# Kernel tuning notes

Hardware: AMD Instinct MI355X
Metric: run time of the kernel (lower is better)

Reference implementation:

```python
import jax, jax.numpy as jnp
import numpy as np

N_NODES = 50000
N_EDGES = 800000
F_IN = 8
H = 128
N_CLASSES = 2


def _gcn_conv(x, W, b, src, dst, n_nodes):
    # PyG GCNConv: add self-loops, symmetric normalization, aggregate, bias.
    h = x @ W  # [N, H]
    loop = jnp.arange(n_nodes, dtype=src.dtype)
    s = jnp.concatenate([src, loop])  # message sources
    d = jnp.concatenate([dst, loop])  # message targets
    deg = jax.ops.segment_sum(jnp.ones_like(s, dtype=h.dtype), d, num_segments=n_nodes)
    dinv = jnp.where(deg > 0, jax.lax.rsqrt(deg), 0.0)
    norm = dinv[s] * dinv[d]  # [E+N]
    out = jax.ops.segment_sum(h[s] * norm[:, None], d, num_segments=n_nodes)
    return out + b


def setup_inputs() -> dict:
    key = jax.random.key(0)
    ks = jax.random.split(key, 10)
    x = jax.random.normal(ks[0], (N_NODES, F_IN), dtype=jnp.float32)
    edge_index = jax.random.randint(ks[1], (2, N_EDGES), 0, N_NODES, dtype=jnp.int64)

    def glorot(k, shape):
        lim = np.sqrt(6.0 / (shape[0] + shape[1]))
        return jax.random.uniform(k, shape, jnp.float32, -lim, lim)

    return {
        "x": x,
        "W1": glorot(ks[2], (F_IN, H)),
        "b1": jnp.zeros((H,), jnp.float32),
        "W2": glorot(ks[3], (H, H)),
        "b2": jnp.zeros((H,), jnp.float32),
        "Wl1": glorot(ks[4], (2 * H, H)),
        "bl1": jnp.zeros((H,), jnp.float32),
        "Wl2": glorot(ks[5], (H, N_CLASSES)),
        "bl2": jnp.zeros((N_CLASSES,), jnp.float32),
        "edge_index": edge_index,
    }


def reference(x, W1, b1, W2, b2, Wl1, bl1, Wl2, bl2, edge_index):
    src, dst = edge_index[0], edge_index[1]
    n = x.shape[0]
    p = jax.nn.relu(_gcn_conv(x, W1, b1, src, dst, n))
    p = jax.nn.relu(_gcn_conv(p, W2, b2, src, dst, n))
    # edge feature: gather endpoints, concat, MLP (Linear-ReLU-Linear), outer ReLU
    e = jnp.concatenate([p[src], p[dst]], axis=1)  # [E, 2H]
    h = jax.nn.relu(e @ Wl1 + bl1)
    out = jax.nn.relu(h @ Wl2 + bl2)  # [E, num_classes]
    return out
```

## Files before the change

kernel.cpp:

```cpp
#include <hip/hip_runtime.h>

#define NN 50000
#define NE 800000
#define F_IN 8
#define H 128
#define BSH 7
#define NB ((NN + 127) >> BSH)
#define EBLK 4096
#define NBE ((NE + EBLK - 1) / EBLK)
#define NP 50048

typedef unsigned int uint;
typedef unsigned short ushort;
typedef __attribute__((ext_vector_type(8))) short short8v;
typedef __attribute__((ext_vector_type(4))) float f32x4;

__device__ __forceinline__ ushort f2bf(float f) {
    uint u = __float_as_uint(f);
    uint r = (u + 0x7fffu + ((u >> 16) & 1u)) >> 16;
    return (ushort)r;
}
__device__ __forceinline__ float bflo(uint u) { return __uint_as_float(u << 16); }
__device__ __forceinline__ float bfhi(uint u) { return __uint_as_float(u & 0xffff0000u); }

__global__ __launch_bounds__(512) void k_hist(const int* __restrict__ dst,
                                              int* __restrict__ Hg) {
    __shared__ int h[NB];
    int t = threadIdx.x, blk = blockIdx.x;
    for (int b = t; b < NB; b += 512) h[b] = 0;
    __syncthreads();
    int e0 = blk * EBLK;
    int e1 = e0 + EBLK; if (e1 > NE) e1 = NE;
    for (int i = e0 + t; i < e1; i += 512) atomicAdd(&h[dst[i] >> BSH], 1);
    __syncthreads();
    for (int b = t; b < NB; b += 512) Hg[blk * NB + b] = h[b];
}

__global__ __launch_bounds__(512) void k_bktscan(const int* __restrict__ Hg,
                                                 int* __restrict__ Bbase) {
    __shared__ int s[512];
    int t = threadIdx.x;
    int acc = 0;
    if (t < NB)
        for (int e = 0; e < NBE; ++e) acc += Hg[e * NB + t];
    s[t] = acc;
    __syncthreads();
    for (int off = 1; off < 512; off <<= 1) {
        int v = (t >= off) ? s[t - off] : 0;
        __syncthreads();
        s[t] += v;
        __syncthreads();
    }
    if (t <= NB) Bbase[t] = (t == 0) ? 0 : s[t - 1];
}

__global__ __launch_bounds__(512) void k_hscan(const int* __restrict__ Bbase,
                                               const int* __restrict__ Hg,
                                               int* __restrict__ Off) {
    int t = threadIdx.x;
    if (t >= NB) return;
    int run = Bbase[t];
    for (int e = 0; e < NBE; ++e) {
        int c = Hg[e * NB + t];
        Off[e * NB + t] = run;
        run += c;
    }
}

__global__ __launch_bounds__(512) void k_scatter(const int* __restrict__ src,
                                                 const int* __restrict__ dst,
                                                 const int* __restrict__ Off,
                                                 int2* __restrict__ bin) {
    __shared__ int cur[NB];
    int t = threadIdx.x, blk = blockIdx.x;
    for (int b = t; b < NB; b += 512) cur[b] = Off[blk * NB + b];
    __syncthreads();
    int e0 = blk * EBLK;
    int e1 = e0 + EBLK; if (e1 > NE) e1 = NE;
    for (int i = e0 + t; i < e1; i += 512) {
        int d = dst[i];
        int b = d >> BSH;
        int pos = atomicAdd(&cur[b], 1);
        bin[pos] = make_int2((src[i] & 0xffff) | ((d & ((1 << BSH) - 1)) << 16), i);
    }
}

__global__ __launch_bounds__(256) void k_binB(const int* __restrict__ Bbase,
                                              const int2* __restrict__ bin,
                                              int2* __restrict__ csr2,
                                              int* __restrict__ rowstart,
                                              float* __restrict__ dinv) {
    int b = blockIdx.x, t = threadIdx.x;
    __shared__ int cnt[128];
    __shared__ int cur[128];
    int base = Bbase[b];
    int end = Bbase[b + 1];
    if (t < 128) cnt[t] = 0;
    __syncthreads();
    for (int idx = base + t; idx < end; idx += 256)
        atomicAdd(&cnt[(uint)bin[idx].x >> 16], 1);
    __syncthreads();
    int myc = (t < 128) ? cnt[t] : 0;
    for (int off = 1; off < 128; off <<= 1) {
        int v = (t >= off && t < 128) ? cnt[t - off] : 0;
        __syncthreads();
        if (t < 128) cnt[t] += v;
        __syncthreads();
    }
    if (t < 128) {
        int startpos = base + cnt[t] - myc;
        int n = (b << BSH) + t;
        if (n < NN) {
            rowstart[n] = startpos;
            dinv[n] = rsqrtf((float)(myc + 1));
        }
        if (b == NB - 1 && t == 127) rowstart[NN] = NE;
        cur[t] = startpos;
    }
    __syncthreads();
    for (int idx = base + t; idx < end; idx += 256) {
        int2 e = bin[idx];
        int ld = (int)((uint)e.x >> 16);
        uint d = (uint)((b << BSH) + ld);
        int pos = atomicAdd(&cur[ld], 1);
        csr2[pos] = make_int2((int)(((uint)e.x & 0xffffu) | (d << 16)), e.y);
    }
}

__global__ __launch_bounds__(256) void k_wcvt(const float* __restrict__ W2,
                                              const float* __restrict__ Wl1,
                                              ushort* __restrict__ Wt2,
                                              ushort* __restrict__ Wtu,
                                              ushort* __restrict__ Wtv) {
    int id = blockIdx.x * 256 + threadIdx.x;
    int m = id >> 14;
    int r = id & 16383;
    int c = r >> 7, k = r & 127;
    float v;
    ushort* dstp;
    if (m == 0)      { v = W2[k * 128 + c];          dstp = Wt2; }
    else if (m == 1) { v = Wl1[k * 128 + c];         dstp = Wtu; }
    else             { v = Wl1[(128 + k) * 128 + c]; dstp = Wtv; }
    dstp[r] = f2bf(v);
}

__global__ __launch_bounds__(256) void k_xw1(const float* __restrict__ x,
                                             const float* __restrict__ W1,
                                             ushort* __restrict__ h) {
    int t = threadIdx.x;
    int n = blockIdx.x * 2 + (t >> 7);
    int j = t & 127;
    const float* xr = x + n * F_IN;
    float acc = 0.f;
#pragma unroll
    for (int k = 0; k < F_IN; ++k) acc += xr[k] * W1[k * H + j];
    h[n * H + j] = f2bf(acc);
}

__global__ __launch_bounds__(256) void k_agg(const ushort* __restrict__ h,
                                             const float* __restrict__ dinv,
                                             const int* __restrict__ rowstart,
                                             const int2* __restrict__ csr2,
                                             const float* __restrict__ bias,
                                             uint* __restrict__ p) {
    int n = blockIdx.x * 4 + (threadIdx.x >> 6);
    int t = threadIdx.x & 63;
    float dn = dinv[n];
    uint us = ((const uint*)(h + (size_t)n * H))[t];
    float w0 = dn * dn;
    float ax = bflo(us) * w0;
    float ay = bfhi(us) * w0;
    int lo = rowstart[n], hi = rowstart[n + 1];
    int i = lo;
    for (; i + 7 < hi; i += 8) {
        int s0 = csr2[i + 0].x & 0xffff;
        int s1 = csr2[i + 1].x & 0xffff;
        int s2 = csr2[i + 2].x & 0xffff;
        int s3 = csr2[i + 3].x & 0xffff;
        int s4 = csr2[i + 4].x & 0xffff;
        int s5 = csr2[i + 5].x & 0xffff;
        int s6 = csr2[i + 6].x & 0xffff;
        int s7 = csr2[i + 7].x & 0xffff;
        uint u0 = ((const uint*)(h + (size_t)s0 * H))[t];
        uint u1 = ((const uint*)(h + (size_t)s1 * H))[t];
        uint u2 = ((const uint*)(h + (size_t)s2 * H))[t];
        uint u3 = ((const uint*)(h + (size_t)s3 * H))[t];
        uint u4 = ((const uint*)(h + (size_t)s4 * H))[t];
        uint u5 = ((const uint*)(h + (size_t)s5 * H))[t];
        uint u6 = ((const uint*)(h + (size_t)s6 * H))[t];
        uint u7 = ((const uint*)(h + (size_t)s7 * H))[t];
        float wa = dinv[s0] * dn, wb = dinv[s1] * dn, wc = dinv[s2] * dn, wd = dinv[s3] * dn;
        float we = dinv[s4] * dn, wf = dinv[s5] * dn, wg = dinv[s6] * dn, wh = dinv[s7] * dn;
        ax += bflo(u0) * wa + bflo(u1) * wb + bflo(u2) * wc + bflo(u3) * wd
            + bflo(u4) * we + bflo(u5) * wf + bflo(u6) * wg + bflo(u7) * wh;
        ay += bfhi(u0) * wa + bfhi(u1) * wb + bfhi(u2) * wc + bfhi(u3) * wd
            + bfhi(u4) * we + bfhi(u5) * wf + bfhi(u6) * wg + bfhi(u7) * wh;
    }
    for (; i < hi; ++i) {
        int s0 = csr2[i].x & 0xffff;
        uint u0 = ((const uint*)(h + (size_t)s0 * H))[t];
        float wa = dinv[s0] * dn;
        ax += bflo(u0) * wa;
        ay += bfhi(u0) * wa;
    }
    float2 bb = ((const float2*)bias)[t];
    ushort rx = f2bf(fmaxf(ax + bb.x, 0.f));
    ushort ry = f2bf(fmaxf(ay + bb.y, 0.f));
    p[(size_t)n * 64 + t] = (uint)rx | ((uint)ry << 16);
}

__global__ __launch_bounds__(256) void k_gmm(const ushort* __restrict__ Xb,
                                             const ushort* __restrict__ Wt,
                                             ushort* __restrict__ Y) {
    __shared__ ushort Ws[16384];
    int t = threadIdx.x;
    for (int i = t; i < 2048; i += 256) {
        int o = i * 16;
        int phys = o ^ (((o >> 8) & 7) << 4);
        *(uint4*)((char*)Ws + phys) = *(const uint4*)((const char*)Wt + o);
    }
    __syncthreads();

    int lane = t & 63;
    int kg = lane >> 4;
    int lr = lane & 15;
    int row0 = blockIdx.x * 128 + (t >> 6) * 32;

    short8v a[2][4];
#pragma unroll
    for (int s = 0; s < 2; ++s)
#pragma unroll
        for (int kk = 0; kk < 4; ++kk)
            a[s][kk] = *(const short8v*)((const char*)Xb +
                ((size_t)(row0 + s * 16 + lr) * 128 + kk * 32 + kg * 8) * 2);

#pragma unroll
    for (int ct = 0; ct < 8; ++ct) {
        int c = ct * 16 + lr;
        f32x4 acc0 = {0.f, 0.f, 0.f, 0.f};
        f32x4 acc1 = {0.f, 0.f, 0.f, 0.f};
#pragma unroll
        for (int kk = 0; kk < 4; ++kk) {
            int o = c * 256 + kk * 64 + kg * 16;
            int phys = o ^ ((c & 7) << 4);
            short8v b = *(const short8v*)((const char*)Ws + phys);
            acc0 = __builtin_amdgcn_mfma_f32_16x16x32_bf16(a[0][kk], b, acc0, 0, 0, 0);
            acc1 = __builtin_amdgcn_mfma_f32_16x16x32_bf16(a[1][kk], b, acc1, 0, 0, 0);
        }
        int colo = ct * 16 + lr;
#pragma unroll
        for (int r = 0; r < 4; ++r) {
            Y[(size_t)(row0 + kg * 4 + r) * 128 + colo] = f2bf(acc0[r]);
            Y[(size_t)(row0 + 16 + kg * 4 + r) * 128 + colo] = f2bf(acc1[r]);
        }
    }
}

#define EPB 128
__global__ __launch_bounds__(256) void k_edge(const int2* __restrict__ csr2,
                                              const ushort* __restrict__ u,
                                              const ushort* __restrict__ v,
                                              const float* __restrict__ bl1,
                                              const float* __restrict__ Wl2,
                                              const float* __restrict__ bl2,
                                              float* __restrict__ out) {
    int g = threadIdx.x >> 4;
    int l16 = threadIdx.x & 15;
    int base = blockIdx.x * EPB + g;

    float4 ba = *(const float4*)(bl1 + l16 * 8);
    float4 bb = *(const float4*)(bl1 + l16 * 8 + 4);
    float4 w0 = *(const float4*)(Wl2 + l16 * 16);
    float4 w1 = *(const float4*)(Wl2 + l16 * 16 + 4);
    float4 w2 = *(const float4*)(Wl2 + l16 * 16 + 8);
    float4 w3 = *(const float4*)(Wl2 + l16 * 16 + 12);
    float b20 = bl2[0], b21 = bl2[1];

    int2 e[8];
#pragma unroll
    for (int j = 0; j < 8; ++j) e[j] = csr2[base + j * 16];
    uint4 uu[8], vv[8];
#pragma unroll
    for (int j = 0; j < 8; ++j) {
        uu[j] = *(const uint4*)((const uint*)(u + (size_t)((uint)e[j].x & 0xffffu) * H) + l16 * 4);
        vv[j] = *(const uint4*)((const uint*)(v + (size_t)((uint)e[j].x >> 16) * H) + l16 * 4);
    }

#pragma unroll
    for (int q = 0; q < 8; ++q) {
        float h0 = fmaxf(bflo(uu[q].x) + bflo(vv[q].x) + ba.x, 0.f);
        float h1 = fmaxf(bfhi(uu[q].x) + bfhi(vv[q].x) + ba.y, 0.f);
        float h2 = fmaxf(bflo(uu[q].y) + bflo(vv[q].y) + ba.z, 0.f);
        float h3 = fmaxf(bfhi(uu[q].y) + bfhi(vv[q].y) + ba.w, 0.f);
        float h4 = fmaxf(bflo(uu[q].z) + bflo(vv[q].z) + bb.x, 0.f);
        float h5 = fmaxf(bfhi(uu[q].z) + bfhi(vv[q].z) + bb.y, 0.f);
        float h6 = fmaxf(bflo(uu[q].w) + bflo(vv[q].w) + bb.z, 0.f);
        float h7 = fmaxf(bfhi(uu[q].w) + bfhi(vv[q].w) + bb.w, 0.f);
        float p0 = h0 * w0.x + h1 * w0.z + h2 * w1.x + h3 * w1.z
                 + h4 * w2.x + h5 * w2.z + h6 * w3.x + h7 * w3.z;
        float p1 = h0 * w0.y + h1 * w0.w + h2 * w1.y + h3 * w1.w
                 + h4 * w2.y + h5 * w2.w + h6 * w3.y + h7 * w3.w;
#pragma unroll
        for (int m = 1; m < 16; m <<= 1) {
            p0 += __shfl_xor(p0, m, 64);
            p1 += __shfl_xor(p1, m, 64);
        }
        if (l16 == 0) {
            float2 o;
            o.x = fmaxf(p0 + b20, 0.f);
            o.y = fmaxf(p1 + b21, 0.f);
            *(float2*)(out + (size_t)e[q].y * 2) = o;
        }
    }
}

extern "C" void kernel_launch(void* const* d_in, const int* in_sizes, int n_in,
                              void* d_out, int out_size, void* d_ws, size_t ws_size,
                              hipStream_t stream) {
    const float* x   = (const float*)d_in[0];
    const float* W1  = (const float*)d_in[1];
    const float* b1  = (const float*)d_in[2];
    const float* W2  = (const float*)d_in[3];
    const float* b2  = (const float*)d_in[4];
    const float* Wl1 = (const float*)d_in[5];
    const float* bl1 = (const float*)d_in[6];
    const float* Wl2 = (const float*)d_in[7];
    const float* bl2 = (const float*)d_in[8];
    const int*   ei  = (const int*)d_in[9];
    const int* src = ei;
    const int* dst = ei + NE;
    float* out = (float*)d_out;

    char* ws = (char*)d_ws;
    size_t off = 0;
    auto alloc = [&](size_t bytes) -> void* {
        void* p = ws + off;
        off = (off + bytes + 255) & ~(size_t)255;
        return p;
    };
    float*  dinv     = (float*)alloc(NN * 4);
    int*    rowstart = (int*)alloc((NN + 1) * 4);
    int*    Bbase    = (int*)alloc((NB + 1) * 4);
    int*    Hg       = (int*)alloc((size_t)NBE * NB * 4);
    int*    Offb     = (int*)alloc((size_t)NBE * NB * 4);
    int2*   csr2     = (int2*)alloc((size_t)NE * 8);
    ushort* hbf      = (ushort*)alloc((size_t)NP * H * 2);
    ushort* pbf      = (ushort*)alloc((size_t)NP * H * 2);
    ushort* ubf      = (ushort*)alloc((size_t)NP * H * 2);
    ushort* vbf      = (ushort*)alloc((size_t)NP * H * 2);
    ushort* Wt2      = (ushort*)alloc(128 * 128 * 2);
    ushort* Wtu      = (ushort*)alloc(128 * 128 * 2);
    ushort* Wtv      = (ushort*)alloc(128 * 128 * 2);
    int2*   bin      = (int2*)ubf;

    k_hist<<<NBE, 512, 0, stream>>>(dst, Hg);
    k_bktscan<<<1, 512, 0, stream>>>(Hg, Bbase);
    k_hscan<<<1, 512, 0, stream>>>(Bbase, Hg, Offb);
    k_scatter<<<NBE, 512, 0, stream>>>(src, dst, Offb, bin);
    k_binB<<<NB, 256, 0, stream>>>(Bbase, bin, csr2, rowstart, dinv);
    k_wcvt<<<192, 256, 0, stream>>>(W2, Wl1, Wt2, Wtu, Wtv);

    k_xw1<<<NN / 2, 256, 0, stream>>>(x, W1, hbf);
    k_agg<<<NN / 4, 256, 0, stream>>>(hbf, dinv, rowstart, csr2, b1, (uint*)pbf);
    k_gmm<<<NP / 128, 256, 0, stream>>>(pbf, Wt2, hbf);
    k_agg<<<NN / 4, 256, 0, stream>>>(hbf, dinv, rowstart, csr2, b2, (uint*)pbf);
    k_gmm<<<NP / 128, 256, 0, stream>>>(pbf, Wtu, ubf);
    k_gmm<<<NP / 128, 256, 0, stream>>>(pbf, Wtv, vbf);
    k_edge<<<NE / EPB, 256, 0, stream>>>(csr2, ubf, vbf, bl1, Wl2, bl2, out);
}
```

Before: 205.8 us.

## Fuse scan kernels, merge u/v GEMMs, software-pipeline persistent edge kernel

Merges the bucket scan and per-block offset scan into a single one-block kernel, saving one launch. Fuses the two output GEMMs that share the same activation input into one kernel holding both weight tiles in LDS, so the activations are read once. Rewrites the edge MLP kernel as a persistent grid of 1250 blocks, each handling 10 chunks of 64 edges with double-buffered register loads, so gathers of the next chunk overlap compute on the current one. This raises register use and cuts the number of resident blocks, which may lower latency hiding.

```diff
diff --git a/kernel.cpp b/kernel.cpp
--- a/kernel.cpp
+++ b/kernel.cpp
@@ -9,6 +9,10 @@
 #define EBLK 4096
 #define NBE ((NE + EBLK - 1) / EBLK)
 #define NP 50048
+#define ECH 64
+#define NCHUNK (NE / ECH)
+#define EGRID 1250
+#define KPB (NCHUNK / EGRID)
 
 typedef unsigned int uint;
 typedef unsigned short ushort;
@@ -36,8 +40,9 @@
     for (int b = t; b < NB; b += 512) Hg[blk * NB + b] = h[b];
 }
 
-__global__ __launch_bounds__(512) void k_bktscan(const int* __restrict__ Hg,
-                                                 int* __restrict__ Bbase) {
+__global__ __launch_bounds__(512) void k_scans(const int* __restrict__ Hg,
+                                               int* __restrict__ Bbase,
+                                               int* __restrict__ Off) {
     __shared__ int s[512];
     int t = threadIdx.x;
     int acc = 0;
@@ -51,19 +56,14 @@
         s[t] += v;
         __syncthreads();
     }
-    if (t <= NB) Bbase[t] = (t == 0) ? 0 : s[t - 1];
-}
-
-__global__ __launch_bounds__(512) void k_hscan(const int* __restrict__ Bbase,
-                                               const int* __restrict__ Hg,
-                                               int* __restrict__ Off) {
-    int t = threadIdx.x;
-    if (t >= NB) return;
-    int run = Bbase[t];
-    for (int e = 0; e < NBE; ++e) {
-        int c = Hg[e * NB + t];
-        Off[e * NB + t] = run;
-        run += c;
+    int base = (t == 0) ? 0 : s[t - 1];
+    if (t <= NB) Bbase[t] = base;
+    if (t < NB) {
+        int run = base;
+        for (int e = 0; e < NBE; ++e) {
+            Off[e * NB + t] = run;
+            run += Hg[e * NB + t];
+        }
     }
 }
 
@@ -220,12 +220,10 @@
         *(uint4*)((char*)Ws + phys) = *(const uint4*)((const char*)Wt + o);
     }
     __syncthreads();
-
     int lane = t & 63;
     int kg = lane >> 4;
     int lr = lane & 15;
     int row0 = blockIdx.x * 128 + (t >> 6) * 32;
-
     short8v a[2][4];
 #pragma unroll
     for (int s = 0; s < 2; ++s)
@@ -233,7 +231,6 @@
         for (int kk = 0; kk < 4; ++kk)
             a[s][kk] = *(const short8v*)((const char*)Xb +
                 ((size_t)(row0 + s * 16 + lr) * 128 + kk * 32 + kg * 8) * 2);
-
 #pragma unroll
     for (int ct = 0; ct < 8; ++ct) {
         int c = ct * 16 + lr;
@@ -256,38 +253,81 @@
     }
 }
 
-#define EPB 128
-__global__ __launch_bounds__(256) void k_edge(const int2* __restrict__ csr2,
-                                              const ushort* __restrict__ u,
-                                              const ushort* __restrict__ v,
-                                              const float* __restrict__ bl1,
-                                              const float* __restrict__ Wl2,
-                                              const float* __restrict__ bl2,
-                                              float* __restrict__ out) {
-    int g = threadIdx.x >> 4;
-    int l16 = threadIdx.x & 15;
-    int base = blockIdx.x * EPB + g;
-
-    float4 ba = *(const float4*)(bl1 + l16 * 8);
-    float4 bb = *(const float4*)(bl1 + l16 * 8 + 4);
-    float4 w0 = *(const float4*)(Wl2 + l16 * 16);
-    float4 w1 = *(const float4*)(Wl2 + l16 * 16 + 4);
-    float4 w2 = *(const float4*)(Wl2 + l16 * 16 + 8);
-    float4 w3 = *(const float4*)(Wl2 + l16 * 16 + 12);
-    float b20 = bl2[0], b21 = bl2[1];
-
-    int2 e[8];
-#pragma unroll
-    for (int j = 0; j < 8; ++j) e[j] = csr2[base + j * 16];
-    uint4 uu[8], vv[8];
-#pragma unroll
-    for (int j = 0; j < 8; ++j) {
+__global__ __launch_bounds__(256) void k_gmm2(const ushort* __restrict__ Xb,
+                                              const ushort* __restrict__ Wtu,
+                                              const ushort* __restrict__ Wtv,
+                                              ushort* __restrict__ Yu,
+                                              ushort* __restrict__ Yv) {
+    __shared__ ushort Ws[2][16384];
+    int t = threadIdx.x;
+    for (int i = t; i < 2048; i += 256) {
+        int o = i * 16;
+        int phys = o ^ (((o >> 8) & 7) << 4);
+        *(uint4*)((char*)Ws[0] + phys) = *(const uint4*)((const char*)Wtu + o);
+        *(uint4*)((char*)Ws[1] + phys) = *(const uint4*)((const char*)Wtv + o);
+    }
+    __syncthreads();
+    int lane = t & 63;
+    int kg = lane >> 4;
+    int lr = lane & 15;
+    int row0 = blockIdx.x * 128 + (t >> 6) * 32;
+    short8v a[2][4];
+#pragma unroll
+    for (int s = 0; s < 2; ++s)
+#pragma unroll
+        for (int kk = 0; kk < 4; ++kk)
+            a[s][kk] = *(const short8v*)((const char*)Xb +
+                ((size_t)(row0 + s * 16 + lr) * 128 + kk * 32 + kg * 8) * 2);
+#pragma unroll
+    for (int ct = 0; ct < 8; ++ct) {
+        int c = ct * 16 + lr;
+        f32x4 au0 = {0.f, 0.f, 0.f, 0.f};
+        f32x4 au1 = {0.f, 0.f, 0.f, 0.f};
+        f32x4 av0 = {0.f, 0.f, 0.f, 0.f};
+        f32x4 av1 = {0.f, 0.f, 0.f, 0.f};
+#pragma unroll
+        for (int kk = 0; kk < 4; ++kk) {
+            int o = c * 256 + kk * 64 + kg * 16;
+            int phys = o ^ ((c & 7) << 4);
+            short8v bu = *(const short8v*)((const char*)Ws[0] + phys);
+            short8v bv = *(const short8v*)((const char*)Ws[1] + phys);
+            au0 = __builtin_amdgcn_mfma_f32_16x16x32_bf16(a[0][kk], bu, au0, 0, 0, 0);
+            au1 = __builtin_amdgcn_mfma_f32_16x16x32_bf16(a[1][kk], bu, au1, 0, 0, 0);
+            av0 = __builtin_amdgcn_mfma_f32_16x16x32_bf16(a[0][kk], bv, av0, 0, 0, 0);
+            av1 = __builtin_amdgcn_mfma_f32_16x16x32_bf16(a[1][kk], bv, av1, 0, 0, 0);
+        }
+        int colo = ct * 16 + lr;
+#pragma unroll
+        for (int r = 0; r < 4; ++r) {
+            Yu[(size_t)(row0 + kg * 4 + r) * 128 + colo] = f2bf(au0[r]);
+            Yu[(size_t)(row0 + 16 + kg * 4 + r) * 128 + colo] = f2bf(au1[r]);
+            Yv[(size_t)(row0 + kg * 4 + r) * 128 + colo] = f2bf(av0[r]);
+            Yv[(size_t)(row0 + 16 + kg * 4 + r) * 128 + colo] = f2bf(av1[r]);
+        }
+    }
+}
+
+__device__ __forceinline__ void edge_load4(const int2* __restrict__ csr2,
+                                           const ushort* __restrict__ u,
+                                           const ushort* __restrict__ v,
+                                           int ch, int g, int l16,
+                                           int2 (&e)[4], uint4 (&uu)[4], uint4 (&vv)[4]) {
+    int bb = ch * ECH + g;
+#pragma unroll
+    for (int j = 0; j < 4; ++j) e[j] = csr2[bb + j * 16];
+#pragma unroll
+    for (int j = 0; j < 4; ++j) {
         uu[j] = *(const uint4*)((const uint*)(u + (size_t)((uint)e[j].x & 0xffffu) * H) + l16 * 4);
         vv[j] = *(const uint4*)((const uint*)(v + (size_t)((uint)e[j].x >> 16) * H) + l16 * 4);
     }
-
-#pragma unroll
-    for (int q = 0; q < 8; ++q) {
+}
+
+__device__ __forceinline__ void edge_comp4(const int2 (&e)[4], const uint4 (&uu)[4], const uint4 (&vv)[4],
+                                           float4 ba, float4 bb, float4 w0, float4 w1,
+                                           float4 w2, float4 w3, float b20, float b21,
+                                           int l16, float* __restrict__ out) {
+#pragma unroll
+    for (int q = 0; q < 4; ++q) {
         float h0 = fmaxf(bflo(uu[q].x) + bflo(vv[q].x) + ba.x, 0.f);
         float h1 = fmaxf(bfhi(uu[q].x) + bfhi(vv[q].x) + ba.y, 0.f);
         float h2 = fmaxf(bflo(uu[q].y) + bflo(vv[q].y) + ba.z, 0.f);
@@ -312,6 +352,41 @@
             *(float2*)(out + (size_t)e[q].y * 2) = o;
         }
     }
+}
+
+__global__ __launch_bounds__(256) void k_edge(const int2* __restrict__ csr2,
+                                              const ushort* __restrict__ u,
+                                              const ushort* __restrict__ v,
+                                              const float* __restrict__ bl1,
+                                              const float* __restrict__ Wl2,
+                                              const float* __restrict__ bl2,
+                                              float* __restrict__ out) {
+    int g = threadIdx.x >> 4;
+    int l16 = threadIdx.x & 15;
+    int c0 = blockIdx.x * KPB;
+
+    float4 ba = *(const float4*)(bl1 + l16 * 8);
+    float4 bb = *(const float4*)(bl1 + l16 * 8 + 4);
+    float4 w0 = *(const float4*)(Wl2 + l16 * 16);
+    float4 w1 = *(const float4*)(Wl2 + l16 * 16 + 4);
+    float4 w2 = *(const float4*)(Wl2 + l16 * 16 + 8);
+    float4 w3 = *(const float4*)(Wl2 + l16 * 16 + 12);
+    float b20 = bl2[0], b21 = bl2[1];
+
+    int2 eA[4], eB[4];
+    uint4 uA[4], vA[4], uB[4], vB[4];
+
+    edge_load4(csr2, u, v, c0, g, l16, eA, uA, vA);
+#pragma unroll 1
+    for (int it = 0; it < (KPB - 2) / 2; ++it) {
+        edge_load4(csr2, u, v, c0 + 2 * it + 1, g, l16, eB, uB, vB);
+        edge_comp4(eA, uA, vA, ba, bb, w0, w1, w2, w3, b20, b21, l16, out);
+        edge_load4(csr2, u, v, c0 + 2 * it + 2, g, l16, eA, uA, vA);
+        edge_comp4(eB, uB, vB, ba, bb, w0, w1, w2, w3, b20, b21, l16, out);
+    }
+    edge_load4(csr2, u, v, c0 + KPB - 1, g, l16, eB, uB, vB);
+    edge_comp4(eA, uA, vA, ba, bb, w0, w1, w2, w3, b20, b21, l16, out);
+    edge_comp4(eB, uB, vB, ba, bb, w0, w1, w2, w3, b20, b21, l16, out);
 }
 
 extern "C" void kernel_launch(void* const* d_in, const int* in_sizes, int n_in,
@@ -354,8 +429,7 @@
     int2*   bin      = (int2*)ubf;
 
     k_hist<<<NBE, 512, 0, stream>>>(dst, Hg);
-    k_bktscan<<<1, 512, 0, stream>>>(Hg, Bbase);
-    k_hscan<<<1, 512, 0, stream>>>(Bbase, Hg, Offb);
+    k_scans<<<1, 512, 0, stream>>>(Hg, Bbase, Offb);
     k_scatter<<<NBE, 512, 0, stream>>>(src, dst, Offb, bin);
     k_binB<<<NB, 256, 0, stream>>>(Bbase, bin, csr2, rowstart, dinv);
     k_wcvt<<<192, 256, 0, stream>>>(W2, Wl1, Wt2, Wtu, Wtv);
@@ -364,7 +438,6 @@
     k_agg<<<NN / 4, 256, 0, stream>>>(hbf, dinv, rowstart, csr2, b1, (uint*)pbf);
     k_gmm<<<NP / 128, 256, 0, stream>>>(pbf, Wt2, hbf);
     k_agg<<<NN / 4, 256, 0, stream>>>(hbf, dinv, rowstart, csr2, b2, (uint*)pbf);
-    k_gmm<<<NP / 128, 256, 0, stream>>>(pbf, Wtu, ubf);
-    k_gmm<<<NP / 128, 256, 0, stream>>>(pbf, Wtv, vbf);
-    k_edge<<<NE / EPB, 256, 0, stream>>>(csr2, ubf, vbf, bl1, Wl2, bl2, out);
-}
+    k_gmm2<<<NP / 128, 256, 0, stream>>>(pbf, Wtu, Wtv, ubf, vbf);
+    k_edge<<<EGRID, 256, 0, stream>>>(csr2, ubf, vbf, bl1, Wl2, bl2, out);
+}
```

Result: no change. 204.4 us (-0.7%).
